# Kernel optimization log

Measured on AMD Instinct MI355X. Metric: run time of the kernel, lower is better.

The kernel has to match this reference:

```python
import jax, jax.numpy as jnp
import numpy as np

D_MODEL = 1024
NHEAD = 16
HEAD_DIM = D_MODEL // NHEAD
D_FF = 4096
EPS = 1e-8


def rmsnorm(x, w):
    # matches torch: norm = ||x||_2 / sqrt(d); out = w * x / (rms + eps)
    rms = jnp.linalg.norm(x, axis=-1, keepdims=True) / np.sqrt(x.shape[-1])
    return w * (x / (rms + EPS))


def setup_inputs() -> dict:
    key = jax.random.key(0)
    ks = jax.random.split(key, 11)
    B, S = 4, 2048
    init = lambda k, shape, fan_in: jax.random.uniform(k, shape, jnp.float32, -1.0, 1.0) / np.sqrt(fan_in)
    return {
        "src": jax.random.normal(ks[0], (B, S, D_MODEL), jnp.float32),
        "qkv_w": init(ks[1], (D_MODEL, 3 * D_MODEL), D_MODEL),
        "qkv_b": init(ks[2], (3 * D_MODEL,), D_MODEL),
        "out_w": init(ks[3], (D_MODEL, D_MODEL), D_MODEL),
        "out_b": init(ks[4], (D_MODEL,), D_MODEL),
        "ff1_w": init(ks[5], (D_MODEL, D_FF), D_MODEL),
        "ff1_b": init(ks[6], (D_FF,), D_MODEL),
        "ff2_w": init(ks[7], (D_FF, D_MODEL), D_FF),
        "ff2_b": init(ks[8], (D_MODEL,), D_FF),
        "norm1_w": jnp.ones((D_MODEL,), jnp.float32),
        "norm2_w": jnp.ones((D_MODEL,), jnp.float32),
    }


def reference(src, qkv_w, qkv_b, out_w, out_b, ff1_w, ff1_b, ff2_w, ff2_b, norm1_w, norm2_w):
    B, S, _ = src.shape
    # --- pre-norm attention block ---
    x = rmsnorm(src, norm1_w)
    qkv = x @ qkv_w + qkv_b                     # [B,S,3*D]
    qkv = qkv.reshape(B, S, 3, NHEAD, HEAD_DIM)
    q, k, v = qkv[:, :, 0], qkv[:, :, 1], qkv[:, :, 2]   # [B,S,H,D]
    scores = jnp.einsum('bshd,bthd->bhst', q, k) / np.sqrt(HEAD_DIM)
    attn = jax.nn.softmax(scores, axis=-1)
    ctx = jnp.einsum('bhst,bthd->bshd', attn, v).reshape(B, S, D_MODEL)
    src = src + ctx @ out_w + out_b
    # --- pre-norm FFN block ---
    y = rmsnorm(src, norm2_w)
    h = jax.nn.gelu(y @ ff1_w + ff1_b, approximate=False)
    src = src + h @ ff2_w + ff2_b
    return src
```

## Files before the change

kernel.cpp:

```cpp
#include <hip/hip_runtime.h>
#include <hip/hip_bf16.h>

#define DM   1024
#define DFF  4096
#define NH   16
#define HD   64
#define SEQ  2048
#define BATCH 4
#define NTOK (BATCH*SEQ)

typedef float  f32x4  __attribute__((ext_vector_type(4)));
typedef short  bf16x8 __attribute__((ext_vector_type(8)));

#define SBAR() asm volatile("s_barrier" ::: "memory")
#define S_VMCNT(N) asm volatile("s_waitcnt vmcnt(" #N ")" ::: "memory")

__device__ __forceinline__ unsigned short f2bf(float f) {
    unsigned int x = __builtin_bit_cast(unsigned int, f);
    x += 0x7fff + ((x >> 16) & 1);
    return (unsigned short)(x >> 16);
}
__device__ __forceinline__ float bf2f(unsigned short u) {
    unsigned int x = (unsigned int)u << 16;
    return __builtin_bit_cast(float, x);
}

__device__ __forceinline__ float fexp2(float x) {
    float r; asm("v_exp_f32 %0, %1" : "=v"(r) : "v"(x)); return r;
}
__device__ __forceinline__ float fmax3(float a, float b, float c) {
    float r; asm("v_max3_f32 %0, %1, %2, %3" : "=v"(r) : "v"(a), "v"(b), "v"(c)); return r;
}

__device__ __forceinline__ void gload_lds16(const void* g, void* l) {
    __builtin_amdgcn_global_load_lds(
        (const __attribute__((address_space(1))) unsigned int*)g,
        (__attribute__((address_space(3))) unsigned int*)l,
        16, 0, 0);
}

__device__ __forceinline__ int swz(int row, int elem) { return elem ^ ((row & 7) << 3); }

__global__ __launch_bounds__(256)
void convT_all(const float* __restrict__ qkv_w, const float* __restrict__ out_w,
               const float* __restrict__ ff1_w, const float* __restrict__ ff2_w,
               unsigned short* __restrict__ qkv_wt, unsigned short* __restrict__ out_wt,
               unsigned short* __restrict__ ff1_wt, unsigned short* __restrict__ ff2_wt)
{
    __shared__ float tile[32][33];
    const float* W; unsigned short* Wt; int K, N, bx, by;
    int b = blockIdx.x;
    if (b < 3072)      { W = qkv_w; Wt = qkv_wt; K = 1024; N = 3072; bx = b % 96;  by = b / 96;  }
    else if (b < 4096) { int i = b - 3072; W = out_w; Wt = out_wt; K = 1024; N = 1024; bx = i % 32;  by = i / 32; }
    else if (b < 8192) { int i = b - 4096; W = ff1_w; Wt = ff1_wt; K = 1024; N = 4096; bx = i % 128; by = i / 128; }
    else               { int i = b - 8192; W = ff2_w; Wt = ff2_wt; K = 4096; N = 1024; bx = i % 32;  by = i / 32; }
    int n0 = bx * 32, k0 = by * 32;
    int tx = threadIdx.x & 31, ty = threadIdx.x >> 5;
    #pragma unroll
    for (int i = 0; i < 4; ++i)
        tile[ty + i*8][tx] = W[(size_t)(k0 + ty + i*8) * N + n0 + tx];
    __syncthreads();
    #pragma unroll
    for (int i = 0; i < 4; ++i)
        Wt[(size_t)(n0 + ty + i*8) * K + k0 + tx] = f2bf(tile[tx][ty + i*8]);
}

template<bool BF16IN>
__global__ __launch_bounds__(256)
void rmsnorm_kernel(const void* __restrict__ inp, const float* __restrict__ w,
                    unsigned short* __restrict__ out)
{
    __shared__ float red[4];
    int row = blockIdx.x, t = threadIdx.x;
    float x0, x1, x2, x3;
    if constexpr (BF16IN) {
        ushort4 u = ((const ushort4*)((const unsigned short*)inp + (size_t)row * DM))[t];
        x0 = bf2f(u.x); x1 = bf2f(u.y); x2 = bf2f(u.z); x3 = bf2f(u.w);
    } else {
        float4 v = ((const float4*)((const float*)inp + (size_t)row * DM))[t];
        x0 = v.x; x1 = v.y; x2 = v.z; x3 = v.w;
    }
    float ss = x0*x0 + x1*x1 + x2*x2 + x3*x3;
    #pragma unroll
    for (int m = 1; m < 64; m <<= 1) ss += __shfl_xor(ss, m);
    if ((t & 63) == 0) red[t >> 6] = ss;
    __syncthreads();
    float tot = red[0] + red[1] + red[2] + red[3];
    float rms = sqrtf(tot) * (1.f / 32.f);
    float inv = 1.f / (rms + 1e-8f);
    float4 wv = ((const float4*)w)[t];
    unsigned int lo = (unsigned int)f2bf(x0*inv*wv.x) | ((unsigned int)f2bf(x1*inv*wv.y) << 16);
    unsigned int hi = (unsigned int)f2bf(x2*inv*wv.z) | ((unsigned int)f2bf(x3*inv*wv.w) << 16);
    uint2 pk; pk.x = lo; pk.y = hi;
    *(uint2*)(out + (size_t)row * DM + t * 4) = pk;
}

template<int MODE, int NB>
__global__ __launch_bounds__(512, 2)
void gemm_tpl(const unsigned short* __restrict__ A,
              const unsigned short* __restrict__ Bt,
              const float* __restrict__ bias,
              int N, int K, int nx,
              const float* __restrict__ residf,
              const unsigned short* __restrict__ residb,
              float* __restrict__ outf,
              unsigned short* __restrict__ outb,
              unsigned short* __restrict__ q,
              unsigned short* __restrict__ kk,
              unsigned short* __restrict__ vt)
{
    constexpr int NJ = NB / 64;
    constexpr int WN = NB / 4;
    __shared__ __align__(16) unsigned short Atile[2][2][256 * 32];
    __shared__ __align__(16) unsigned short Btile[2][2][NB * 32];
    const int tid = threadIdx.x, w = tid >> 6, l = tid & 63;
    const int lr = l & 15, lh = l >> 4;
    const int wm = w >> 2, wn = w & 3;
    const int nwg = gridDim.x, cpx = nwg >> 3;
    const int sid = (blockIdx.x & 7) * cpx + (blockIdx.x >> 3);
    const int by = sid / nx, bx = sid - by * nx;
    const int m0 = by * 256, n0 = bx * NB;
    const int nkt = K >> 6;
    const int srow = w * 16 + (l >> 2);
    const int scol = (((l & 3) ^ (srow & 3)) << 3);

    auto stageA = [&](int kt, int ks, int half, int bi) {
        int r0 = half * 128;
        gload_lds16(A + (size_t)(m0 + r0 + srow) * K + kt * 64 + ks * 32 + scol,
                    &Atile[bi][ks][(r0 + w * 16) * 32]);
    };
    auto stageB = [&](int kt, int ks, int half, int bi) {
        int r0 = half * 128;
        gload_lds16(Bt + (size_t)(n0 + r0 + srow) * K + kt * 64 + ks * 32 + scol,
                    &Btile[bi][ks][(r0 + w * 16) * 32]);
    };

    f32x4 acc[8][NJ];
    #pragma unroll
    for (int a = 0; a < 8; ++a)
        #pragma unroll
        for (int j = 0; j < NJ; ++j) acc[a][j] = {0.f, 0.f, 0.f, 0.f};

    #pragma unroll
    for (int ks = 0; ks < 2; ++ks) {
        stageA(0, ks, 0, 0); stageA(0, ks, 1, 0);
        stageB(0, ks, 0, 0);
        if (NB == 256) stageB(0, ks, 1, 0);
    }

    int bi = 0;
    for (int t = 0; t < nkt; ++t) {
        #pragma unroll
        for (int ks = 0; ks < 2; ++ks) {
            if (ks == 0 || t + 1 < nkt) {
                if constexpr (NB == 256) { S_VMCNT(4); } else { S_VMCNT(3); }
            } else {
                S_VMCNT(0);
            }
            SBAR();
            bf16x8 bB[NJ];
            #pragma unroll
            for (int j = 0; j < NJ; ++j) {
                int row = wn * WN + j * 16 + lr;
                bB[j] = *(const bf16x8*)&Btile[bi][ks][row * 32 + ((lh ^ (row & 3)) << 3)];
            }
            #pragma unroll
            for (int rho = 0; rho < 2; ++rho) {
                bf16x8 aA[4];
                #pragma unroll
                for (int i = 0; i < 4; ++i) {
                    int row = wm * 128 + rho * 64 + i * 16 + lr;
                    aA[i] = *(const bf16x8*)&Atile[bi][ks][row * 32 + ((lh ^ (row & 3)) << 3)];
                }
                if (t + 1 < nkt) {
                    if (rho == 0) { stageA(t + 1, ks, 0, bi ^ 1); stageA(t + 1, ks, 1, bi ^ 1); }
                    else          { stageB(t + 1, ks, 0, bi ^ 1);
                                    if (NB == 256) stageB(t + 1, ks, 1, bi ^ 1); }
                }
                SBAR();
                __builtin_amdgcn_s_setprio(1);
                #pragma unroll
                for (int i = 0; i < 4; ++i)
                    #pragma unroll
                    for (int j = 0; j < NJ; ++j)
                        acc[rho * 4 + i][j] = __builtin_amdgcn_mfma_f32_16x16x32_bf16(
                            aA[i], bB[j], acc[rho * 4 + i][j], 0, 0, 0);
                __builtin_amdgcn_s_setprio(0);
            }
        }
        bi ^= 1;
    }

    #pragma unroll
    for (int a = 0; a < 8; ++a) {
        const int rho = a >> 2, i = a & 3;
        #pragma unroll
        for (int j = 0; j < NJ; ++j) {
            #pragma unroll
            for (int r = 0; r < 4; ++r) {
                int row = m0 + wm * 128 + rho * 64 + i * 16 + lh * 4 + r;
                int col = n0 + wn * WN + j * 16 + lr;
                float v = acc[a][j][r] + bias[col];
                if (MODE == 0) {
                    int wh = col >> 10, h = (col >> 6) & 15, d = col & 63;
                    int b = row >> 11, s = row & 2047;
                    size_t base = (size_t)(b * NH + h);
                    if (wh == 0)      q [(base * SEQ + s) * HD + d] = f2bf(v * 0.18033688f);
                    else if (wh == 1) kk[(base * SEQ + s) * HD + d] = f2bf(v);
                    else              vt[(base * HD + d) * SEQ + s] = f2bf(v);
                } else if (MODE == 2) {
                    float g = 0.5f * v * (1.f + erff(v * 0.70710678118f));
                    outb[(size_t)row * N + col] = f2bf(g);
                } else if (MODE == 3) {
                    outf[(size_t)row * N + col] = v + bf2f(residb[(size_t)row * N + col]);
                } else {
                    outb[(size_t)row * N + col] = f2bf(v + residf[(size_t)row * N + col]);
                }
            }
        }
    }
}

__global__ __launch_bounds__(256, 3)
void attn_kernel(const unsigned short* __restrict__ q,
                 const unsigned short* __restrict__ k,
                 const unsigned short* __restrict__ vt,
                 unsigned short* __restrict__ ctx)
{
    __shared__ __align__(16) unsigned short Ks[2][64 * 64];
    __shared__ __align__(16) unsigned short Vs[2][64 * 64];
    __shared__ __align__(16) unsigned short PQ[4][32 * 64];

    const int tid = threadIdx.x, w = tid >> 6, l = tid & 63;
    const int lr = l & 15, lh = l >> 4;

    const int sid = (blockIdx.x & 7) * 128 + (blockIdx.x >> 3);
    const int bh = sid >> 4, qt = sid & 15;
    const int b = bh >> 4, h = bh & 15;

    const int rloc = l >> 3;
    const int cswz = (((l & 7) ^ rloc) << 3);

    const unsigned short* kbase0 = k  + (size_t)bh * SEQ * HD;
    const unsigned short* vbase0 = vt + (size_t)bh * HD * SEQ;
    const int NT = SEQ / 64;

    auto stageK = [&](int t, int buf) {
        const unsigned short* kb = kbase0 + (size_t)t * 64 * HD;
        #pragma unroll
        for (int c = 0; c < 2; ++c) {
            int r0 = (w * 2 + c) * 8;
            gload_lds16(kb + (size_t)(r0 + rloc) * HD + cswz, &Ks[buf][r0 * 64]);
        }
    };
    auto stageV = [&](int t, int buf) {
        const unsigned short* vb = vbase0 + t * 64;
        #pragma unroll
        for (int c = 0; c < 2; ++c) {
            int d0 = w * 16 + c * 8;
            gload_lds16(vb + (size_t)(d0 + rloc) * SEQ + cswz, &Vs[buf][d0 * 64]);
        }
    };

    unsigned short* Pw = &PQ[w][0];
    const unsigned short* qbase = q + ((size_t)bh * SEQ + qt * 128 + w * 32) * HD;
    #pragma unroll
    for (int c = 0; c < 4; ++c) {
        int r0 = c * 8;
        gload_lds16(qbase + (size_t)(r0 + rloc) * HD + cswz, &Pw[r0 * 64]);
    }
    stageK(0, 0);
    stageV(0, 0);
    S_VMCNT(4);
    bf16x8 aq[2][2];
    #pragma unroll
    for (int g = 0; g < 2; ++g) {
        int row = g * 16 + lr;
        aq[g][0] = *(const bf16x8*)&Pw[row * 64 + swz(row,      lh * 8)];
        aq[g][1] = *(const bf16x8*)&Pw[row * 64 + swz(row, 32 + lh * 8)];
    }
    __syncthreads();

    float mrow[2] = {-1e30f, -1e30f}, lrow[2] = {0.f, 0.f};
    f32x4 o[2][4];
    #pragma unroll
    for (int g = 0; g < 2; ++g)
        #pragma unroll
        for (int nf = 0; nf < 4; ++nf) o[g][nf] = {0.f, 0.f, 0.f, 0.f};

    for (int t = 0; t < NT; ++t) {
        const int cur = t & 1;
        if (t + 1 < NT) { stageK(t + 1, cur ^ 1); stageV(t + 1, cur ^ 1); }

        const unsigned short* Kc = &Ks[cur][0];
        const unsigned short* Vc = &Vs[cur][0];

        f32x4 sc[2][4];
        __builtin_amdgcn_s_setprio(1);
        #pragma unroll
        for (int j = 0; j < 4; ++j) {
            int kr = j * 16 + lr;
            bf16x8 kb0 = *(const bf16x8*)&Kc[kr * 64 + swz(kr,      lh * 8)];
            bf16x8 kb1 = *(const bf16x8*)&Kc[kr * 64 + swz(kr, 32 + lh * 8)];
            #pragma unroll
            for (int g = 0; g < 2; ++g) {
                f32x4 z = {0.f, 0.f, 0.f, 0.f};
                z = __builtin_amdgcn_mfma_f32_16x16x32_bf16(kb0, aq[g][0], z, 0, 0, 0);
                z = __builtin_amdgcn_mfma_f32_16x16x32_bf16(kb1, aq[g][1], z, 0, 0, 0);
                sc[g][j] = z;
            }
        }
        __builtin_amdgcn_s_setprio(0);

        #pragma unroll
        for (int g = 0; g < 2; ++g) {
            float mt = fmax3(sc[g][0][0], sc[g][0][1], sc[g][0][2]);
            mt = fmax3(mt, sc[g][0][3], sc[g][1][0]);
            mt = fmax3(mt, sc[g][1][1], sc[g][1][2]);
            mt = fmax3(mt, sc[g][1][3], sc[g][2][0]);
            mt = fmax3(mt, sc[g][2][1], sc[g][2][2]);
            mt = fmax3(mt, sc[g][2][3], sc[g][3][0]);
            mt = fmax3(mt, sc[g][3][1], sc[g][3][2]);
            mt = fmaxf(mt, sc[g][3][3]);
            mt = fmaxf(mt, __shfl_xor(mt, 16));
            mt = fmaxf(mt, __shfl_xor(mt, 32));

            float al = 1.f;
            if (!__all(mt <= mrow[g] + 8.f)) {
                float mnew = fmaxf(mrow[g], mt);
                al = fexp2(mrow[g] - mnew);
                mrow[g] = mnew;
                float alo[4];
                #pragma unroll
                for (int r = 0; r < 4; ++r) alo[r] = __shfl(al, lh * 4 + r);
                #pragma unroll
                for (int nf = 0; nf < 4; ++nf)
                    #pragma unroll
                    for (int r = 0; r < 4; ++r) o[g][nf][r] *= alo[r];
            }

            float rs = 0.f;
            int prow = g * 16 + lr;
            #pragma unroll
            for (int j = 0; j < 4; ++j) {
                float p0 = fexp2(sc[g][j][0] - mrow[g]), p1 = fexp2(sc[g][j][1] - mrow[g]);
                float p2 = fexp2(sc[g][j][2] - mrow[g]), p3 = fexp2(sc[g][j][3] - mrow[g]);
                rs += (p0 + p1) + (p2 + p3);
                unsigned int w0, w1;
                asm("v_cvt_pk_bf16_f32 %0, %1, %2" : "=v"(w0) : "v"(p0), "v"(p1));
                asm("v_cvt_pk_bf16_f32 %0, %1, %2" : "=v"(w1) : "v"(p2), "v"(p3));
                int k0 = j * 16 + lh * 4;
                int e = prow * 64 + (k0 ^ ((prow & 7) << 3));
                *(unsigned int*)&Pw[e]     = w0;
                *(unsigned int*)&Pw[e + 2] = w1;
            }
            rs += __shfl_xor(rs, 16);
            rs += __shfl_xor(rs, 32);
            lrow[g] = lrow[g] * al + rs;
        }

        bf16x8 ap[2][2];
        #pragma unroll
        for (int g = 0; g < 2; ++g) {
            int prow = g * 16 + lr;
            ap[g][0] = *(const bf16x8*)&Pw[prow * 64 + swz(prow,      lh * 8)];
            ap[g][1] = *(const bf16x8*)&Pw[prow * 64 + swz(prow, 32 + lh * 8)];
        }

        __builtin_amdgcn_s_setprio(1);
        #pragma unroll
        for (int nf = 0; nf < 4; ++nf) {
            int vr = nf * 16 + lr;
            bf16x8 vb0 = *(const bf16x8*)&Vc[vr * 64 + swz(vr,      lh * 8)];
            bf16x8 vb1 = *(const bf16x8*)&Vc[vr * 64 + swz(vr, 32 + lh * 8)];
            #pragma unroll
            for (int g = 0; g < 2; ++g) {
                o[g][nf] = __builtin_amdgcn_mfma_f32_16x16x32_bf16(ap[g][0], vb0, o[g][nf], 0, 0, 0);
                o[g][nf] = __builtin_amdgcn_mfma_f32_16x16x32_bf16(ap[g][1], vb1, o[g][nf], 0, 0, 0);
            }
        }
        __builtin_amdgcn_s_setprio(0);

        __syncthreads();
    }

    #pragma unroll
    for (int g = 0; g < 2; ++g) {
        float linv = 1.f / lrow[g];
        float lo4[4];
        #pragma unroll
        for (int r = 0; r < 4; ++r) lo4[r] = __shfl(linv, lh * 4 + r);
        #pragma unroll
        for (int nf = 0; nf < 4; ++nf)
            #pragma unroll
            for (int r = 0; r < 4; ++r) {
                int row = qt * 128 + w * 32 + g * 16 + lh * 4 + r;
                ctx[((size_t)b * SEQ + row) * DM + h * 64 + nf * 16 + lr] =
                    f2bf(o[g][nf][r] * lo4[r]);
            }
    }
}

extern "C" void kernel_launch(void* const* d_in, const int* in_sizes, int n_in,
                              void* d_out, int out_size, void* d_ws, size_t ws_size,
                              hipStream_t stream)
{
    const float* src   = (const float*)d_in[0];
    const float* qkv_w = (const float*)d_in[1];
    const float* qkv_b = (const float*)d_in[2];
    const float* out_w = (const float*)d_in[3];
    const float* out_b = (const float*)d_in[4];
    const float* ff1_w = (const float*)d_in[5];
    const float* ff1_b = (const float*)d_in[6];
    const float* ff2_w = (const float*)d_in[7];
    const float* ff2_b = (const float*)d_in[8];
    const float* n1_w  = (const float*)d_in[9];
    const float* n2_w  = (const float*)d_in[10];

    char* ws = (char*)d_ws;
    const size_t MB = 1u << 20;
    unsigned short* qkv_wt = (unsigned short*)(ws);
    unsigned short* out_wt = (unsigned short*)(ws + 6*MB);
    unsigned short* ff1_wt = (unsigned short*)(ws + 8*MB);
    unsigned short* ff2_wt = (unsigned short*)(ws + 16*MB);
    unsigned short* xb     = (unsigned short*)(ws + 24*MB);
    unsigned short* qb     = (unsigned short*)(ws + 40*MB);
    unsigned short* kb     = (unsigned short*)(ws + 56*MB);
    unsigned short* vtb    = (unsigned short*)(ws + 72*MB);
    unsigned short* hb     = (unsigned short*)(ws + 24*MB);
    unsigned short* ctxb   = (unsigned short*)(ws + 88*MB);
    unsigned short* yb     = (unsigned short*)(ws + 88*MB);
    unsigned short* src2b  = (unsigned short*)(ws + 104*MB);
    float* outp = (float*)d_out;

    convT_all<<<12288, 256, 0, stream>>>(qkv_w, out_w, ff1_w, ff2_w,
                                         qkv_wt, out_wt, ff1_wt, ff2_wt);

    rmsnorm_kernel<false><<<NTOK, 256, 0, stream>>>(src, n1_w, xb);

    gemm_tpl<0, 128><<<768, 512, 0, stream>>>(xb, qkv_wt, qkv_b, 3072, 1024, 24,
                                              nullptr, nullptr, nullptr, nullptr, qb, kb, vtb);

    attn_kernel<<<SEQ/128 * BATCH*NH, 256, 0, stream>>>(qb, kb, vtb, ctxb);

    gemm_tpl<4, 128><<<256, 512, 0, stream>>>(ctxb, out_wt, out_b, 1024, 1024, 8,
                                              src, nullptr, nullptr, src2b, nullptr, nullptr, nullptr);

    rmsnorm_kernel<true><<<NTOK, 256, 0, stream>>>(src2b, n2_w, yb);

    gemm_tpl<2, 256><<<512, 512, 0, stream>>>(yb, ff1_wt, ff1_b, 4096, 1024, 16,
                                              nullptr, nullptr, nullptr, hb, nullptr, nullptr, nullptr);

    gemm_tpl<3, 128><<<256, 512, 0, stream>>>(hb, ff2_wt, ff2_b, 1024, 4096, 8,
                                              nullptr, src2b, outp, nullptr, nullptr, nullptr, nullptr);
}
```

Measured before the change: 450.8 us.

## Enlarge attention query tile, compute row sums via MFMA, approximate GELU with tanh form

The attention kernel now handles 256 query rows per block (64 per wave) instead of 128, so each staged K/V tile is reused across twice as many queries. The grid is halved and occupancy is lowered to 2 blocks. Softmax row sums are now accumulated with an MFMA against a ones vector, which removes the shuffle reductions. Separately, the exact erf GELU in the FF1 epilogue is replaced by a tanh-style sigmoid approximation using exp2 and rcp; this changes numerics and risks going beyond the accuracy tolerance.

```diff
diff --git a/kernel.cpp b/kernel.cpp
--- a/kernel.cpp
+++ b/kernel.cpp
@@ -27,6 +27,9 @@
 
 __device__ __forceinline__ float fexp2(float x) {
     float r; asm("v_exp_f32 %0, %1" : "=v"(r) : "v"(x)); return r;
+}
+__device__ __forceinline__ float frcp(float x) {
+    float r; asm("v_rcp_f32 %0, %1" : "=v"(r) : "v"(x)); return r;
 }
 __device__ __forceinline__ float fmax3(float a, float b, float c) {
     float r; asm("v_max3_f32 %0, %1, %2, %3" : "=v"(r) : "v"(a), "v"(b), "v"(c)); return r;
@@ -209,7 +212,11 @@
                     else if (wh == 1) kk[(base * SEQ + s) * HD + d] = f2bf(v);
                     else              vt[(base * HD + d) * SEQ + s] = f2bf(v);
                 } else if (MODE == 2) {
-                    float g = 0.5f * v * (1.f + erff(v * 0.70710678118f));
+                    float x = v;
+                    float t2 = fmaf(x * x * x, 0.044715f, x);
+                    float av = fminf(t2 * 2.3022079f, 80.f);
+                    float u = fexp2(av);
+                    float g = x * u * frcp(u + 1.f);
                     outb[(size_t)row * N + col] = f2bf(g);
                 } else if (MODE == 3) {
                     outf[(size_t)row * N + col] = v + bf2f(residb[(size_t)row * N + col]);
@@ -221,7 +228,7 @@
     }
 }
 
-__global__ __launch_bounds__(256, 3)
+__global__ __launch_bounds__(256, 2)
 void attn_kernel(const unsigned short* __restrict__ q,
                  const unsigned short* __restrict__ k,
                  const unsigned short* __restrict__ vt,
@@ -229,13 +236,13 @@
 {
     __shared__ __align__(16) unsigned short Ks[2][64 * 64];
     __shared__ __align__(16) unsigned short Vs[2][64 * 64];
-    __shared__ __align__(16) unsigned short PQ[4][32 * 64];
+    __shared__ __align__(16) unsigned short PQ[4][64 * 64];
 
     const int tid = threadIdx.x, w = tid >> 6, l = tid & 63;
     const int lr = l & 15, lh = l >> 4;
 
-    const int sid = (blockIdx.x & 7) * 128 + (blockIdx.x >> 3);
-    const int bh = sid >> 4, qt = sid & 15;
+    const int sid = (blockIdx.x & 7) * 64 + (blockIdx.x >> 3);
+    const int bh = sid >> 3, qt = sid & 7;
     const int b = bh >> 4, h = bh & 15;
 
     const int rloc = l >> 3;
@@ -263,30 +270,37 @@
     };
 
     unsigned short* Pw = &PQ[w][0];
-    const unsigned short* qbase = q + ((size_t)bh * SEQ + qt * 128 + w * 32) * HD;
-    #pragma unroll
-    for (int c = 0; c < 4; ++c) {
+    const unsigned short* qbase = q + ((size_t)bh * SEQ + qt * 256 + w * 64) * HD;
+    #pragma unroll
+    for (int c = 0; c < 8; ++c) {
         int r0 = c * 8;
         gload_lds16(qbase + (size_t)(r0 + rloc) * HD + cswz, &Pw[r0 * 64]);
     }
     stageK(0, 0);
     stageV(0, 0);
     S_VMCNT(4);
-    bf16x8 aq[2][2];
-    #pragma unroll
-    for (int g = 0; g < 2; ++g) {
+    bf16x8 aq[4][2];
+    #pragma unroll
+    for (int g = 0; g < 4; ++g) {
         int row = g * 16 + lr;
         aq[g][0] = *(const bf16x8*)&Pw[row * 64 + swz(row,      lh * 8)];
         aq[g][1] = *(const bf16x8*)&Pw[row * 64 + swz(row, 32 + lh * 8)];
     }
     __syncthreads();
 
-    float mrow[2] = {-1e30f, -1e30f}, lrow[2] = {0.f, 0.f};
-    f32x4 o[2][4];
-    #pragma unroll
-    for (int g = 0; g < 2; ++g)
+    bf16x8 vone;
+    #pragma unroll
+    for (int i = 0; i < 8; ++i) vone[i] = (short)0x3F80;
+
+    float mrow[4] = {-1e30f, -1e30f, -1e30f, -1e30f};
+    f32x4 lacc[4];
+    f32x4 o[4][4];
+    #pragma unroll
+    for (int g = 0; g < 4; ++g) {
+        lacc[g] = {0.f, 0.f, 0.f, 0.f};
         #pragma unroll
         for (int nf = 0; nf < 4; ++nf) o[g][nf] = {0.f, 0.f, 0.f, 0.f};
+    }
 
     for (int t = 0; t < NT; ++t) {
         const int cur = t & 1;
@@ -295,86 +309,88 @@
         const unsigned short* Kc = &Ks[cur][0];
         const unsigned short* Vc = &Vs[cur][0];
 
-        f32x4 sc[2][4];
-        __builtin_amdgcn_s_setprio(1);
+        bf16x8 kb[4][2];
         #pragma unroll
         for (int j = 0; j < 4; ++j) {
             int kr = j * 16 + lr;
-            bf16x8 kb0 = *(const bf16x8*)&Kc[kr * 64 + swz(kr,      lh * 8)];
-            bf16x8 kb1 = *(const bf16x8*)&Kc[kr * 64 + swz(kr, 32 + lh * 8)];
-            #pragma unroll
-            for (int g = 0; g < 2; ++g) {
+            kb[j][0] = *(const bf16x8*)&Kc[kr * 64 + swz(kr,      lh * 8)];
+            kb[j][1] = *(const bf16x8*)&Kc[kr * 64 + swz(kr, 32 + lh * 8)];
+        }
+
+        #pragma unroll
+        for (int g = 0; g < 4; ++g) {
+            f32x4 sc[4];
+            __builtin_amdgcn_s_setprio(1);
+            #pragma unroll
+            for (int j = 0; j < 4; ++j) {
                 f32x4 z = {0.f, 0.f, 0.f, 0.f};
-                z = __builtin_amdgcn_mfma_f32_16x16x32_bf16(kb0, aq[g][0], z, 0, 0, 0);
-                z = __builtin_amdgcn_mfma_f32_16x16x32_bf16(kb1, aq[g][1], z, 0, 0, 0);
-                sc[g][j] = z;
-            }
-        }
-        __builtin_amdgcn_s_setprio(0);
-
-        #pragma unroll
-        for (int g = 0; g < 2; ++g) {
-            float mt = fmax3(sc[g][0][0], sc[g][0][1], sc[g][0][2]);
-            mt = fmax3(mt, sc[g][0][3], sc[g][1][0]);
-            mt = fmax3(mt, sc[g][1][1], sc[g][1][2]);
-            mt = fmax3(mt, sc[g][1][3], sc[g][2][0]);
-            mt = fmax3(mt, sc[g][2][1], sc[g][2][2]);
-            mt = fmax3(mt, sc[g][2][3], sc[g][3][0]);
-            mt = fmax3(mt, sc[g][3][1], sc[g][3][2]);
-            mt = fmaxf(mt, sc[g][3][3]);
+                z = __builtin_amdgcn_mfma_f32_16x16x32_bf16(kb[j][0], aq[g][0], z, 0, 0, 0);
+                z = __builtin_amdgcn_mfma_f32_16x16x32_bf16(kb[j][1], aq[g][1], z, 0, 0, 0);
+                sc[j] = z;
+            }
+            __builtin_amdgcn_s_setprio(0);
+
+            float mt = fmax3(sc[0][0], sc[0][1], sc[0][2]);
+            mt = fmax3(mt, sc[0][3], sc[1][0]);
+            mt = fmax3(mt, sc[1][1], sc[1][2]);
+            mt = fmax3(mt, sc[1][3], sc[2][0]);
+            mt = fmax3(mt, sc[2][1], sc[2][2]);
+            mt = fmax3(mt, sc[2][3], sc[3][0]);
+            mt = fmax3(mt, sc[3][1], sc[3][2]);
+            mt = fmaxf(mt, sc[3][3]);
             mt = fmaxf(mt, __shfl_xor(mt, 16));
             mt = fmaxf(mt, __shfl_xor(mt, 32));
 
-            float al = 1.f;
             if (!__all(mt <= mrow[g] + 8.f)) {
                 float mnew = fmaxf(mrow[g], mt);
-                al = fexp2(mrow[g] - mnew);
+                float al = fexp2(mrow[g] - mnew);
                 mrow[g] = mnew;
                 float alo[4];
                 #pragma unroll
                 for (int r = 0; r < 4; ++r) alo[r] = __shfl(al, lh * 4 + r);
                 #pragma unroll
-                for (int nf = 0; nf < 4; ++nf)
+                for (int r = 0; r < 4; ++r) {
+                    lacc[g][r] *= alo[r];
                     #pragma unroll
-                    for (int r = 0; r < 4; ++r) o[g][nf][r] *= alo[r];
-            }
-
-            float rs = 0.f;
+                    for (int nf = 0; nf < 4; ++nf) o[g][nf][r] *= alo[r];
+                }
+            }
+
             int prow = g * 16 + lr;
             #pragma unroll
             for (int j = 0; j < 4; ++j) {
-                float p0 = fexp2(sc[g][j][0] - mrow[g]), p1 = fexp2(sc[g][j][1] - mrow[g]);
-                float p2 = fexp2(sc[g][j][2] - mrow[g]), p3 = fexp2(sc[g][j][3] - mrow[g]);
-                rs += (p0 + p1) + (p2 + p3);
+                float p0 = fexp2(sc[j][0] - mrow[g]), p1 = fexp2(sc[j][1] - mrow[g]);
+                float p2 = fexp2(sc[j][2] - mrow[g]), p3 = fexp2(sc[j][3] - mrow[g]);
                 unsigned int w0, w1;
                 asm("v_cvt_pk_bf16_f32 %0, %1, %2" : "=v"(w0) : "v"(p0), "v"(p1));
                 asm("v_cvt_pk_bf16_f32 %0, %1, %2" : "=v"(w1) : "v"(p2), "v"(p3));
                 int k0 = j * 16 + lh * 4;
                 int e = prow * 64 + (k0 ^ ((prow & 7) << 3));
-                *(unsigned int*)&Pw[e]     = w0;
-                *(unsigned int*)&Pw[e + 2] = w1;
-            }
-            rs += __shfl_xor(rs, 16);
-            rs += __shfl_xor(rs, 32);
-            lrow[g] = lrow[g] * al + rs;
-        }
-
-        bf16x8 ap[2][2];
-        #pragma unroll
-        for (int g = 0; g < 2; ++g) {
+                uint2 pk; pk.x = w0; pk.y = w1;
+                *(uint2*)&Pw[e] = pk;
+            }
+        }
+
+        bf16x8 ap[4][2];
+        #pragma unroll
+        for (int g = 0; g < 4; ++g) {
             int prow = g * 16 + lr;
             ap[g][0] = *(const bf16x8*)&Pw[prow * 64 + swz(prow,      lh * 8)];
             ap[g][1] = *(const bf16x8*)&Pw[prow * 64 + swz(prow, 32 + lh * 8)];
         }
-
         __builtin_amdgcn_s_setprio(1);
+        #pragma unroll
+        for (int g = 0; g < 4; ++g) {
+            lacc[g] = __builtin_amdgcn_mfma_f32_16x16x32_bf16(ap[g][0], vone, lacc[g], 0, 0, 0);
+            lacc[g] = __builtin_amdgcn_mfma_f32_16x16x32_bf16(ap[g][1], vone, lacc[g], 0, 0, 0);
+        }
         #pragma unroll
         for (int nf = 0; nf < 4; ++nf) {
             int vr = nf * 16 + lr;
             bf16x8 vb0 = *(const bf16x8*)&Vc[vr * 64 + swz(vr,      lh * 8)];
             bf16x8 vb1 = *(const bf16x8*)&Vc[vr * 64 + swz(vr, 32 + lh * 8)];
             #pragma unroll
-            for (int g = 0; g < 2; ++g) {
+            for (int g = 0; g < 4; ++g) {
                 o[g][nf] = __builtin_amdgcn_mfma_f32_16x16x32_bf16(ap[g][0], vb0, o[g][nf], 0, 0, 0);
                 o[g][nf] = __builtin_amdgcn_mfma_f32_16x16x32_bf16(ap[g][1], vb1, o[g][nf], 0, 0, 0);
             }
@@ -385,18 +401,17 @@
     }
 
     #pragma unroll
-    for (int g = 0; g < 2; ++g) {
-        float linv = 1.f / lrow[g];
-        float lo4[4];
-        #pragma unroll
-        for (int r = 0; r < 4; ++r) lo4[r] = __shfl(linv, lh * 4 + r);
+    for (int g = 0; g < 4; ++g) {
+        float linv[4];
+        #pragma unroll
+        for (int r = 0; r < 4; ++r) linv[r] = frcp(lacc[g][r]);
         #pragma unroll
         for (int nf = 0; nf < 4; ++nf)
             #pragma unroll
             for (int r = 0; r < 4; ++r) {
-                int row = qt * 128 + w * 32 + g * 16 + lh * 4 + r;
+                int row = qt * 256 + w * 64 + g * 16 + lh * 4 + r;
                 ctx[((size_t)b * SEQ + row) * DM + h * 64 + nf * 16 + lr] =
-                    f2bf(o[g][nf][r] * lo4[r]);
+                    f2bf(o[g][nf][r] * linv[r]);
             }
     }
 }
@@ -441,7 +456,7 @@
     gemm_tpl<0, 128><<<768, 512, 0, stream>>>(xb, qkv_wt, qkv_b, 3072, 1024, 24,
                                               nullptr, nullptr, nullptr, nullptr, qb, kb, vtb);
 
-    attn_kernel<<<SEQ/128 * BATCH*NH, 256, 0, stream>>>(qb, kb, vtb, ctxb);
+    attn_kernel<<<SEQ/256 * BATCH*NH, 256, 0, stream>>>(qb, kb, vtb, ctxb);
 
     gemm_tpl<4, 128><<<256, 512, 0, stream>>>(ctxb, out_wt, out_b, 1024, 1024, 8,
                                               src, nullptr, nullptr, src2b, nullptr, nullptr, nullptr);
```

New measurement: 414.5 us. 8.0% less time.
